# Performance work log

Hardware: AMD Instinct MI355X
Metric: run time of the kernel (lower is better)

Reference implementation:

```python
import jax, jax.numpy as jnp
import numpy as np

B, FNP, D = 16, 4096, 512
P, S, F = 16, 8, 32

def setup_inputs() -> dict:
    key = jax.random.key(0)
    k1, k2 = jax.random.split(key)
    token_states = jax.random.normal(k1, (B, FNP, D), dtype=jnp.float32)
    W = jax.random.normal(k2, (2 * P, D), dtype=jnp.float32) * 0.02
    b = jnp.zeros((2 * P,), dtype=jnp.float32)
    return {"token_states": token_states, "W": W, "b": b, "T": 1032}

def reference(token_states, W, b, T):
    Bsz, FNp, Dm = token_states.shape
    Np = FNp // F
    h = token_states.reshape(Bsz, F, Np, Dm)
    # per-patch linear head: [B, F, Np, 2P]
    raw = jnp.einsum('bfnd,ed->bfne', h, W) + b
    raw = raw.reshape(Bsz, F, Np, 2, P)
    mu = raw[:, :, :, 0, :]                                   # [B, F, Np, P]
    sigma = jnp.clip(jnp.exp(raw[:, :, :, 1, :]), 1e-06, None)
    mu = jnp.transpose(mu, (0, 2, 3, 1))                      # [B, Np, P, F]
    sigma = jnp.transpose(sigma, (0, 2, 3, 1))
    # overlap-add fold: time index for each (patch, offset)
    t = (jnp.arange(Np)[:, None] * S + jnp.arange(P)[None, :]).reshape(-1)  # [Np*P]
    valid = (t < T)
    t_c = jnp.where(valid, t, 0)
    vmask = valid.astype(mu.dtype)[None, :, None]             # [1, Np*P, 1]
    mu_flat = mu.reshape(Bsz, Np * P, F) * vmask
    sg_flat = sigma.reshape(Bsz, Np * P, F) * vmask
    mu_full = jnp.zeros((Bsz, T, F), dtype=mu.dtype).at[:, t_c, :].add(mu_flat)
    sigma_full = jnp.zeros((Bsz, T, F), dtype=mu.dtype).at[:, t_c, :].add(sg_flat)
    counts = jnp.zeros((T,), dtype=mu.dtype).at[t_c].add(valid.astype(mu.dtype))
    counts = jnp.clip(counts, 1.0, None)[None, :, None]       # [1, T, 1]
    return (mu_full / counts, sigma_full / counts)
```

## Files before the change

### kernel.cpp

```cpp
#include <hip/hip_runtime.h>
#include <math.h>

#define B_    16
#define F_    32
#define NP_   128
#define D_    512
#define P_    16
#define KC    32
#define NCH   16
#define BUFW  (NP_ * KC)
#define NRING 8
#define EOFF  (NRING * BUFW)

typedef __attribute__((ext_vector_type(8)))  short  short8;
typedef __attribute__((ext_vector_type(16))) float  floatx16;

union Frag { short8 v; unsigned int u[4]; };

__device__ inline unsigned int cvt_pk_bf16(float lo, float hi) {
    unsigned int r;
    asm volatile("v_cvt_pk_bf16_f32 %0, %1, %2" : "=v"(r) : "v"(lo), "v"(hi));
    return r;
}

#define EBAR asm volatile("s_waitcnt lgkmcnt(0)\n\ts_barrier" ::: "memory")

__global__ __launch_bounds__(512, 2)
void pd_kernel(const float* __restrict__ ts,
               const float* __restrict__ W,
               const float* __restrict__ bias,
               float* __restrict__ out, int T)
{
    __shared__ float smem[EOFF + NP_ * 33];

    const int tid  = threadIdx.x;
    const int lane = tid & 63;
    const int wave = tid >> 6;
    const int mt   = wave & 3;
    const int p    = wave >> 2;

    const int d  = blockIdx.x;
    const int b  = (d & 7) | (((d >> 7) & 1) << 3);
    const int fp = (d >> 3) & 15;
    const float* __restrict__ tsb0 = ts + ((size_t)(b * F_ + 2 * fp) * NP_) * D_;
    const float* __restrict__ tsb1 = tsb0 + (size_t)NP_ * D_;

    auto STAGE = [&](const float* base, int cc) {
#pragma unroll
        for (int it = 0; it < 2; ++it) {
            const int slot = it * 512 + tid;
            const int r2 = slot >> 3;
            const int qg = (slot & 7) ^ (r2 & 7);
            const float* src = base + r2 * D_ + cc * KC + (qg << 2);
            float* dst = smem + (cc & 7) * BUFW + (slot << 2);
            __builtin_amdgcn_global_load_lds(
                (const __attribute__((address_space(1))) unsigned int*)src,
                (__attribute__((address_space(3))) unsigned int*)dst,
                16, 0, 0);
        }
    };

    STAGE(tsb0, 0);
    STAGE(tsb0, 1);
    __builtin_amdgcn_sched_barrier(0);

    const int e_b = lane & 31;
    const int kh  = lane >> 5;
    Frag bf[NCH];
    {
        const float* wb = W + (size_t)e_b * D_ + kh * 8;
#pragma unroll
        for (int c = 0; c < NCH; ++c) {
            const int k = c * 32 + p * 16;
            const float4 lo = *(const float4*)(wb + k);
            const float4 hi = *(const float4*)(wb + k + 4);
            bf[c].u[0] = cvt_pk_bf16(lo.x, lo.y);
            bf[c].u[1] = cvt_pk_bf16(lo.z, lo.w);
            bf[c].u[2] = cvt_pk_bf16(hi.x, hi.y);
            bf[c].u[3] = cvt_pk_bf16(hi.z, hi.w);
        }
    }
    __builtin_amdgcn_sched_barrier(0);

#pragma unroll
    for (int c = 2; c < 7; ++c) STAGE(tsb0, c);
    __builtin_amdgcn_sched_barrier(0);

    const int ldsrow = mt * 32 + (lane & 31);
    const int sw8    = ldsrow & 7;
    const int aq     = p * 4 + kh * 2;

    const int TF = T * F_;
    const size_t halfoff = (size_t)B_ * TF;
    float* const E = smem + EOFF;

    auto COMPUTE = [&](int c, floatx16& acc) {
        const float* rowp = smem + (c & 7) * BUFW + ldsrow * KC;
        const float4 lo = *(const float4*)(rowp + ((aq ^ sw8) << 2));
        const float4 hi = *(const float4*)(rowp + (((aq + 1) ^ sw8) << 2));
        Frag a;
        a.u[0] = cvt_pk_bf16(lo.x, lo.y);
        a.u[1] = cvt_pk_bf16(lo.z, lo.w);
        a.u[2] = cvt_pk_bf16(hi.x, hi.y);
        a.u[3] = cvt_pk_bf16(hi.z, hi.w);
        acc = __builtin_amdgcn_mfma_f32_32x32x16_bf16(a.v, bf[c].v, acc, 0, 0, 0);
    };

    floatx16 accA, accB;
#pragma unroll
    for (int r = 0; r < 16; ++r) { accA[r] = 0.f; accB[r] = 0.f; }

#pragma unroll
    for (int c = 0; c < NCH; ++c) {
        asm volatile("s_waitcnt vmcnt(12)\n\ts_barrier" ::: "memory");
        __builtin_amdgcn_sched_barrier(0);
        if (c <= 8) STAGE(tsb0, c + 7);
        else        STAGE(tsb1, c - 9);
        __builtin_amdgcn_sched_barrier(0);
        COMPUTE(c, accA);
    }

    const int f0 = 2 * fp;
    const int QT = (2 * T + 3) / 4;
#pragma unroll
    for (int c = 0; c < NCH; ++c) {
        if (c <= 9)
            asm volatile("s_waitcnt vmcnt(12) lgkmcnt(0)\n\ts_barrier" ::: "memory");
        else if (c == 10)
            asm volatile("s_waitcnt vmcnt(10)\n\ts_barrier" ::: "memory");
        else if (c == 11)
            asm volatile("s_waitcnt vmcnt(8)\n\ts_barrier" ::: "memory");
        else if (c == 12)
            asm volatile("s_waitcnt vmcnt(6)\n\ts_barrier" ::: "memory");
        else if (c == 13)
            asm volatile("s_waitcnt vmcnt(4)\n\ts_barrier" ::: "memory");
        else if (c == 14)
            asm volatile("s_waitcnt vmcnt(2)\n\ts_barrier" ::: "memory");
        else
            asm volatile("s_waitcnt vmcnt(0)\n\ts_barrier" ::: "memory");
        __builtin_amdgcn_sched_barrier(0);

        if (c <= 8) STAGE(tsb1, c + 7);
        __builtin_amdgcn_sched_barrier(0);

        if (c == 0) {
            if (p == 0) {
#pragma unroll
                for (int r = 0; r < 16; ++r) {
                    const int rowl = (r & 3) + 8 * (r >> 2) + 4 * kh;
                    E[(mt * 32 + rowl) * 33 + e_b] = accA[r];
                }
            }
        } else if (c == 1) {
            if (p == 1) {
#pragma unroll
                for (int r = 0; r < 16; ++r) {
                    const int rowl = (r & 3) + 8 * (r >> 2) + 4 * kh;
                    E[(mt * 32 + rowl) * 33 + e_b] += accA[r];
                }
            }
        } else if (c == 2) {
#pragma unroll
            for (int jj = 0; jj < 8; ++jj) {
                const int item = tid * 8 + jj;
                const int n = item >> 5;
                const int e = item & 31;
                float v = E[n * 33 + e] + bias[e];
                if (e >= P_) v = fmaxf(expf(v), 1e-6f);
                E[n * 33 + e] = v;
            }
        } else if (c >= 3 && c <= 6) {
            const int g  = c - 3;
            const int hi = min((g + 1) * QT, 2 * T);
            for (int item = g * QT + tid; item < hi; item += 512) {
                const int half = (item >= T) ? 1 : 0;
                const int t    = item - half * T;
                const int nmax = min(NP_ - 1, t >> 3);
                const int nmin = (t > 8) ? ((t - 8) >> 3) : 0;
                float sum = 0.f;
                const int cnt = nmax - nmin + 1;
                for (int nn = nmin; nn <= nmax; ++nn)
                    sum += E[nn * 33 + (half << 4) + (t - (nn << 3))];
                const float r = (cnt > 0) ? sum / (float)cnt : 0.f;
                out[(size_t)half * halfoff + (size_t)b * TF + (size_t)t * F_ + f0] = r;
            }
        }

        COMPUTE(c, accB);
    }

    const int f1 = 2 * fp + 1;
    if (p == 0) {
#pragma unroll
        for (int r = 0; r < 16; ++r) {
            const int rowl = (r & 3) + 8 * (r >> 2) + 4 * kh;
            E[(mt * 32 + rowl) * 33 + e_b] = accB[r];
        }
    }
    EBAR;
    if (p == 1) {
#pragma unroll
        for (int r = 0; r < 16; ++r) {
            const int rowl = (r & 3) + 8 * (r >> 2) + 4 * kh;
            E[(mt * 32 + rowl) * 33 + e_b] += accB[r];
        }
    }
    EBAR;
#pragma unroll
    for (int jj = 0; jj < 8; ++jj) {
        const int item = tid * 8 + jj;
        const int n = item >> 5;
        const int e = item & 31;
        float v = E[n * 33 + e] + bias[e];
        if (e >= P_) v = fmaxf(expf(v), 1e-6f);
        E[n * 33 + e] = v;
    }
    EBAR;
    for (int item = tid; item < 2 * T; item += 512) {
        const int half = (item >= T) ? 1 : 0;
        const int t    = item - half * T;
        const int nmax = min(NP_ - 1, t >> 3);
        const int nmin = (t > 8) ? ((t - 8) >> 3) : 0;
        float sum = 0.f;
        const int cnt = nmax - nmin + 1;
        for (int nn = nmin; nn <= nmax; ++nn)
            sum += E[nn * 33 + (half << 4) + (t - (nn << 3))];
        const float r = (cnt > 0) ? sum / (float)cnt : 0.f;
        out[(size_t)half * halfoff + (size_t)b * TF + (size_t)t * F_ + f1] = r;
    }
}

extern "C" void kernel_launch(void* const* d_in, const int* in_sizes, int n_in,
                              void* d_out, int out_size, void* d_ws, size_t ws_size,
                              hipStream_t stream)
{
    const float* ts   = (const float*)d_in[0];
    const float* W    = (const float*)d_in[1];
    const float* bias = (const float*)d_in[2];
    float* out = (float*)d_out;

    const int T = out_size / (2 * B_ * F_);

    dim3 grid(B_ * F_ / 2);
    dim3 block(512);
    pd_kernel<<<grid, block, 0, stream>>>(ts, W, bias, out, T);
}
```

Measured before the change: 37.16 us.

## Double K-chunk width with 4-deep ring and fuse bias/exp into accumulator reduce

New measurement: 36.69 us. No clear change (-1.3%).

```diff
diff --git a/kernel.cpp b/kernel.cpp
--- a/kernel.cpp
+++ b/kernel.cpp
@@ -6,10 +6,10 @@
 #define NP_   128
 #define D_    512
 #define P_    16
-#define KC    32
-#define NCH   16
+#define KC    64
+#define NCH   8
 #define BUFW  (NP_ * KC)
-#define NRING 8
+#define NRING 4
 #define EOFF  (NRING * BUFW)
 
 typedef __attribute__((ext_vector_type(8)))  short  short8;
@@ -47,12 +47,12 @@
 
     auto STAGE = [&](const float* base, int cc) {
 #pragma unroll
-        for (int it = 0; it < 2; ++it) {
+        for (int it = 0; it < 4; ++it) {
             const int slot = it * 512 + tid;
-            const int r2 = slot >> 3;
-            const int qg = (slot & 7) ^ (r2 & 7);
+            const int r2 = slot >> 4;
+            const int qg = (slot & 15) ^ (r2 & 15);
             const float* src = base + r2 * D_ + cc * KC + (qg << 2);
-            float* dst = smem + (cc & 7) * BUFW + (slot << 2);
+            float* dst = smem + (cc & 3) * BUFW + (slot << 2);
             __builtin_amdgcn_global_load_lds(
                 (const __attribute__((address_space(1))) unsigned int*)src,
                 (__attribute__((address_space(3))) unsigned int*)dst,
@@ -66,28 +66,29 @@
 
     const int e_b = lane & 31;
     const int kh  = lane >> 5;
-    Frag bf[NCH];
+    Frag bf[NCH][2];
     {
         const float* wb = W + (size_t)e_b * D_ + kh * 8;
 #pragma unroll
-        for (int c = 0; c < NCH; ++c) {
-            const int k = c * 32 + p * 16;
-            const float4 lo = *(const float4*)(wb + k);
-            const float4 hi = *(const float4*)(wb + k + 4);
-            bf[c].u[0] = cvt_pk_bf16(lo.x, lo.y);
-            bf[c].u[1] = cvt_pk_bf16(lo.z, lo.w);
-            bf[c].u[2] = cvt_pk_bf16(hi.x, hi.y);
-            bf[c].u[3] = cvt_pk_bf16(hi.z, hi.w);
-        }
+        for (int c = 0; c < NCH; ++c)
+#pragma unroll
+            for (int j = 0; j < 2; ++j) {
+                const int k = (4 * c + p + 2 * j) * 16;
+                const float4 lo = *(const float4*)(wb + k);
+                const float4 hi = *(const float4*)(wb + k + 4);
+                bf[c][j].u[0] = cvt_pk_bf16(lo.x, lo.y);
+                bf[c][j].u[1] = cvt_pk_bf16(lo.z, lo.w);
+                bf[c][j].u[2] = cvt_pk_bf16(hi.x, hi.y);
+                bf[c][j].u[3] = cvt_pk_bf16(hi.z, hi.w);
+            }
     }
     __builtin_amdgcn_sched_barrier(0);
 
-#pragma unroll
-    for (int c = 2; c < 7; ++c) STAGE(tsb0, c);
+    STAGE(tsb0, 2);
     __builtin_amdgcn_sched_barrier(0);
 
     const int ldsrow = mt * 32 + (lane & 31);
-    const int sw8    = ldsrow & 7;
+    const int sw16   = ldsrow & 15;
     const int aq     = p * 4 + kh * 2;
 
     const int TF = T * F_;
@@ -95,15 +96,19 @@
     float* const E = smem + EOFF;
 
     auto COMPUTE = [&](int c, floatx16& acc) {
-        const float* rowp = smem + (c & 7) * BUFW + ldsrow * KC;
-        const float4 lo = *(const float4*)(rowp + ((aq ^ sw8) << 2));
-        const float4 hi = *(const float4*)(rowp + (((aq + 1) ^ sw8) << 2));
-        Frag a;
-        a.u[0] = cvt_pk_bf16(lo.x, lo.y);
-        a.u[1] = cvt_pk_bf16(lo.z, lo.w);
-        a.u[2] = cvt_pk_bf16(hi.x, hi.y);
-        a.u[3] = cvt_pk_bf16(hi.z, hi.w);
-        acc = __builtin_amdgcn_mfma_f32_32x32x16_bf16(a.v, bf[c].v, acc, 0, 0, 0);
+        const float* rowp = smem + (c & 3) * BUFW + ldsrow * KC;
+#pragma unroll
+        for (int j = 0; j < 2; ++j) {
+            const int q0 = aq + j * 8;
+            const float4 lo = *(const float4*)(rowp + ((q0 ^ sw16) << 2));
+            const float4 hi = *(const float4*)(rowp + (((q0 + 1) ^ sw16) << 2));
+            Frag a;
+            a.u[0] = cvt_pk_bf16(lo.x, lo.y);
+            a.u[1] = cvt_pk_bf16(lo.z, lo.w);
+            a.u[2] = cvt_pk_bf16(hi.x, hi.y);
+            a.u[3] = cvt_pk_bf16(hi.z, hi.w);
+            acc = __builtin_amdgcn_mfma_f32_32x32x16_bf16(a.v, bf[c][j].v, acc, 0, 0, 0);
+        }
     };
 
     floatx16 accA, accB;
@@ -112,10 +117,10 @@
 
 #pragma unroll
     for (int c = 0; c < NCH; ++c) {
-        asm volatile("s_waitcnt vmcnt(12)\n\ts_barrier" ::: "memory");
-        __builtin_amdgcn_sched_barrier(0);
-        if (c <= 8) STAGE(tsb0, c + 7);
-        else        STAGE(tsb1, c - 9);
+        asm volatile("s_waitcnt vmcnt(8)\n\ts_barrier" ::: "memory");
+        __builtin_amdgcn_sched_barrier(0);
+        if (c <= 4) STAGE(tsb0, c + 3);
+        else        STAGE(tsb1, c - 5);
         __builtin_amdgcn_sched_barrier(0);
         COMPUTE(c, accA);
     }
@@ -124,23 +129,17 @@
     const int QT = (2 * T + 3) / 4;
 #pragma unroll
     for (int c = 0; c < NCH; ++c) {
-        if (c <= 9)
-            asm volatile("s_waitcnt vmcnt(12) lgkmcnt(0)\n\ts_barrier" ::: "memory");
-        else if (c == 10)
-            asm volatile("s_waitcnt vmcnt(10)\n\ts_barrier" ::: "memory");
-        else if (c == 11)
-            asm volatile("s_waitcnt vmcnt(8)\n\ts_barrier" ::: "memory");
-        else if (c == 12)
-            asm volatile("s_waitcnt vmcnt(6)\n\ts_barrier" ::: "memory");
-        else if (c == 13)
-            asm volatile("s_waitcnt vmcnt(4)\n\ts_barrier" ::: "memory");
-        else if (c == 14)
-            asm volatile("s_waitcnt vmcnt(2)\n\ts_barrier" ::: "memory");
+        if (c <= 4)
+            asm volatile("s_waitcnt vmcnt(8) lgkmcnt(0)\n\ts_barrier" ::: "memory");
+        else if (c == 5)
+            asm volatile("s_waitcnt vmcnt(8) lgkmcnt(0)\n\ts_barrier" ::: "memory");
+        else if (c == 6)
+            asm volatile("s_waitcnt vmcnt(4) lgkmcnt(0)\n\ts_barrier" ::: "memory");
         else
-            asm volatile("s_waitcnt vmcnt(0)\n\ts_barrier" ::: "memory");
-        __builtin_amdgcn_sched_barrier(0);
-
-        if (c <= 8) STAGE(tsb1, c + 7);
+            asm volatile("s_waitcnt vmcnt(0) lgkmcnt(0)\n\ts_barrier" ::: "memory");
+        __builtin_amdgcn_sched_barrier(0);
+
+        if (c <= 4) STAGE(tsb1, c + 3);
         __builtin_amdgcn_sched_barrier(0);
 
         if (c == 0) {
@@ -156,21 +155,13 @@
 #pragma unroll
                 for (int r = 0; r < 16; ++r) {
                     const int rowl = (r & 3) + 8 * (r >> 2) + 4 * kh;
-                    E[(mt * 32 + rowl) * 33 + e_b] += accA[r];
+                    float v = E[(mt * 32 + rowl) * 33 + e_b] + accA[r] + bias[e_b];
+                    if (e_b >= P_) v = fmaxf(expf(v), 1e-6f);
+                    E[(mt * 32 + rowl) * 33 + e_b] = v;
                 }
             }
-        } else if (c == 2) {
-#pragma unroll
-            for (int jj = 0; jj < 8; ++jj) {
-                const int item = tid * 8 + jj;
-                const int n = item >> 5;
-                const int e = item & 31;
-                float v = E[n * 33 + e] + bias[e];
-                if (e >= P_) v = fmaxf(expf(v), 1e-6f);
-                E[n * 33 + e] = v;
-            }
-        } else if (c >= 3 && c <= 6) {
-            const int g  = c - 3;
+        } else if (c >= 2 && c <= 5) {
+            const int g  = c - 2;
             const int hi = min((g + 1) * QT, 2 * T);
             for (int item = g * QT + tid; item < hi; item += 512) {
                 const int half = (item >= T) ? 1 : 0;
@@ -202,18 +193,10 @@
 #pragma unroll
         for (int r = 0; r < 16; ++r) {
             const int rowl = (r & 3) + 8 * (r >> 2) + 4 * kh;
-            E[(mt * 32 + rowl) * 33 + e_b] += accB[r];
-        }
-    }
-    EBAR;
-#pragma unroll
-    for (int jj = 0; jj < 8; ++jj) {
-        const int item = tid * 8 + jj;
-        const int n = item >> 5;
-        const int e = item & 31;
-        float v = E[n * 33 + e] + bias[e];
-        if (e >= P_) v = fmaxf(expf(v), 1e-6f);
-        E[n * 33 + e] = v;
+            float v = E[(mt * 32 + rowl) * 33 + e_b] + accB[r] + bias[e_b];
+            if (e_b >= P_) v = fmaxf(expf(v), 1e-6f);
+            E[(mt * 32 + rowl) * 33 + e_b] = v;
+        }
     }
     EBAR;
     for (int item = tid; item < 2 * T; item += 512) {
```
